# Kernel tuning notes

Hardware: AMD Instinct MI355X
Metric: run time of the kernel (lower is better)

Reference implementation:

```python
import jax, jax.numpy as jnp
import numpy as np

N_EMBD = 1024
N_HEAD = 16
HEAD_DIM = N_EMBD // N_HEAD


def setup_inputs() -> dict:
    key = jax.random.key(0)
    ks = jax.random.split(key, 5)
    B, T, C = 2, 2048, N_EMBD
    scale = 0.02
    return {
        "x": jax.random.normal(ks[0], (B, T, C), dtype=jnp.float32),
        "w_attn": jax.random.normal(ks[1], (C, 3 * C), dtype=jnp.float32) * scale,
        "b_attn": jax.random.normal(ks[2], (3 * C,), dtype=jnp.float32) * scale,
        "w_proj": jax.random.normal(ks[3], (C, C), dtype=jnp.float32) * scale,
        "b_proj": jax.random.normal(ks[4], (C,), dtype=jnp.float32) * scale,
    }


def reference(x, w_attn, b_attn, w_proj, b_proj):
    B, T, C = x.shape
    H, D = N_HEAD, HEAD_DIM
    qkv = x @ w_attn + b_attn  # [B,T,3C]
    q, k, v = jnp.split(qkv, 3, axis=-1)
    # [B,T,C] -> [B,H,T,D]
    q = q.reshape(B, T, H, D).transpose(0, 2, 1, 3)
    k = k.reshape(B, T, H, D).transpose(0, 2, 1, 3)
    v = v.reshape(B, T, H, D).transpose(0, 2, 1, 3)
    scores = jnp.einsum("bhqd,bhkd->bhqk", q, k) / jnp.sqrt(jnp.float32(D))
    causal = jnp.tril(jnp.ones((T, T), dtype=bool))
    scores = jnp.where(causal, scores, jnp.finfo(scores.dtype).min)
    attn = jax.nn.softmax(scores, axis=-1)
    y = jnp.einsum("bhqk,bhkd->bhqd", attn, v)  # [B,H,T,D]
    y = y.transpose(0, 2, 1, 3).reshape(B, T, C)
    return y @ w_proj + b_proj
```

## Files before the change

### kernel.cpp

```cpp
#include <hip/hip_runtime.h>

typedef unsigned short u16;
typedef u16 u16x4 __attribute__((ext_vector_type(4)));
typedef u16 u16x8 __attribute__((ext_vector_type(8)));
typedef __bf16 bf16x8 __attribute__((ext_vector_type(8)));
typedef float floatx4 __attribute__((ext_vector_type(4)));

#define N_EMBD 1024
#define N_HEAD 16
#define HEAD_DIM 64
#define SEQ 2048
#define BATCH 2
#define M_ROWS (BATCH * SEQ)

typedef __attribute__((address_space(1))) const unsigned char ga_t;
typedef __attribute__((address_space(3))) unsigned char la_t;

#if __has_builtin(__builtin_amdgcn_exp2f)
#define EXP2(x) __builtin_amdgcn_exp2f(x)
#else
#define EXP2(x) exp2f(x)
#endif

__device__ __forceinline__ u16 cvt_bf16(float f) {
  return __builtin_bit_cast(u16, (__bf16)f);
}

__global__ __launch_bounds__(256) void prep(const float* __restrict__ x,
                                            u16* __restrict__ xb,
                                            const float* __restrict__ wa,
                                            const float* __restrict__ wp,
                                            u16* __restrict__ outa,
                                            u16* __restrict__ outp) {
  const int bid = blockIdx.x;
  if (bid < 2048) {
    const long i = ((long)bid * 256 + threadIdx.x) * 8;
    const float4 f0 = *(const float4*)&x[i];
    const float4 f1 = *(const float4*)&x[i + 4];
    u16x8 p;
    p[0] = cvt_bf16(f0.x); p[1] = cvt_bf16(f0.y);
    p[2] = cvt_bf16(f0.z); p[3] = cvt_bf16(f0.w);
    p[4] = cvt_bf16(f1.x); p[5] = cvt_bf16(f1.y);
    p[6] = cvt_bf16(f1.z); p[7] = cvt_bf16(f1.w);
    *(u16x8*)&xb[i] = p;
    return;
  }
  __shared__ u16 tile[32][33];
  const int t = bid - 2048;
  const int gx = t & 127;
  const int gy = t >> 7;
  const int R = N_EMBD;
  const float* in;
  u16* out;
  int C, bx;
  if (gx < 96) {
    in = wa; out = outa; C = 3 * N_EMBD; bx = gx * 32;
  } else {
    in = wp; out = outp; C = N_EMBD; bx = (gx - 96) * 32;
  }
  const int by = gy * 32;
  const int tx = threadIdx.x & 31;
  const int ty = threadIdx.x >> 5;
#pragma unroll
  for (int j = 0; j < 32; j += 8)
    tile[ty + j][tx] = cvt_bf16(in[(long)(by + ty + j) * C + bx + tx]);
  __syncthreads();
#pragma unroll
  for (int j = 0; j < 32; j += 8)
    out[(long)(bx + ty + j) * R + by + tx] = tile[tx][ty + j];
}

#define BK 32

template <int MODE>
__device__ __forceinline__ void stage128(const u16* __restrict__ A,
                                         const u16* __restrict__ Bt, int bm,
                                         int bn, int kt, int K, int tid,
                                         u16* as, u16* bs) {
  const int w = tid >> 6;
  const int l = tid & 63;
  const int lrow = l >> 2;
#pragma unroll
  for (int p = 0; p < 2; ++p) {
    const int arow = p * 64 + w * 16;
    const int row = arow + lrow;
    const int sl = (l & 3) ^ ((row >> 1) & 3);
    long gA;
    if (MODE == 0) {
      gA = (long)(bm + row) * K + kt + sl * 8;
    } else {
      const int m = bm + row;
      const int b = m >> 11, t = m & 2047;
      const int k0 = kt + sl * 8;
      const int head = k0 >> 6, dd = k0 & 63;
      gA = (((long)(b * N_HEAD + head)) * SEQ + t) * HEAD_DIM + dd;
    }
    __builtin_amdgcn_global_load_lds((ga_t*)(A + gA), (la_t*)&as[arow * BK],
                                     16, 0, 0);
    const long gB = (long)(bn + row) * K + kt + sl * 8;
    __builtin_amdgcn_global_load_lds((ga_t*)(Bt + gB), (la_t*)&bs[arow * BK],
                                     16, 0, 0);
  }
}

template <int MODE>
__global__ __launch_bounds__(256) void gemm128(
    const u16* __restrict__ A, const u16* __restrict__ Bt,
    const float* __restrict__ bias, float* __restrict__ out,
    u16* __restrict__ qo, u16* __restrict__ ko, u16* __restrict__ vo, int N,
    int K) {
  __shared__ u16 As[2][128 * BK];
  __shared__ u16 Bs[2][128 * BK];
  const int tid = threadIdx.x;

  const int nx = gridDim.x;
  const int nwg = nx * gridDim.y;
  int lin = blockIdx.y * nx + blockIdx.x;
  lin = (lin & 7) * (nwg >> 3) + (lin >> 3);
  const int bm = (lin / nx) * 128;
  const int bn = (lin % nx) * 128;

  const int w = tid >> 6;
  const int l = tid & 63;
  const int wm = (w >> 1) * 64;
  const int wn = (w & 1) * 64;
  const int m16 = l & 15;
  const int quad = l >> 4;
  const int ksw = (quad ^ ((m16 >> 1) & 3)) * 8;

  floatx4 acc[4][4];
#pragma unroll
  for (int i = 0; i < 4; ++i)
#pragma unroll
    for (int j = 0; j < 4; ++j) acc[i][j] = (floatx4){0.f, 0.f, 0.f, 0.f};

  const int nk = K / BK;
  stage128<MODE>(A, Bt, bm, bn, 0, K, tid, As[0], Bs[0]);
  __syncthreads();

  int cur = 0;
  for (int t = 0; t < nk; ++t) {
    if (t + 1 < nk)
      stage128<MODE>(A, Bt, bm, bn, (t + 1) * BK, K, tid, As[cur ^ 1],
                     Bs[cur ^ 1]);

    bf16x8 af[4], bfr[4];
#pragma unroll
    for (int i = 0; i < 4; ++i)
      af[i] = __builtin_bit_cast(
          bf16x8, *(const u16x8*)&As[cur][(wm + i * 16 + m16) * BK + ksw]);
#pragma unroll
    for (int j = 0; j < 4; ++j)
      bfr[j] = __builtin_bit_cast(
          bf16x8, *(const u16x8*)&Bs[cur][(wn + j * 16 + m16) * BK + ksw]);
#pragma unroll
    for (int i = 0; i < 4; ++i)
#pragma unroll
      for (int j = 0; j < 4; ++j)
        acc[i][j] = __builtin_amdgcn_mfma_f32_16x16x32_bf16(af[i], bfr[j],
                                                            acc[i][j], 0, 0, 0);
    __syncthreads();
    cur ^= 1;
  }

#pragma unroll
  for (int i = 0; i < 4; ++i) {
#pragma unroll
    for (int j = 0; j < 4; ++j) {
      const int col = bn + wn + j * 16 + m16;
      const float bv = bias[col];
      if (MODE == 1) {
#pragma unroll
        for (int r = 0; r < 4; ++r) {
          const int row = bm + wm + i * 16 + quad * 4 + r;
          out[(long)row * N_EMBD + col] = acc[i][j][r] + bv;
        }
      } else {
        const int which = col >> 10;
        const int cc = col & 1023;
        const int h = cc >> 6;
        const int dd = cc & 63;
        const int row0 = bm + wm + i * 16 + quad * 4;
        const int b = row0 >> 11;
        const int t0 = row0 & 2047;
        if (which == 2) {
          u16x4 pk;
#pragma unroll
          for (int r = 0; r < 4; ++r) pk[r] = cvt_bf16(acc[i][j][r] + bv);
          *(u16x4*)&vo[(((long)(b * N_HEAD + h)) * HEAD_DIM + dd) * SEQ + t0] =
              pk;
        } else {
          u16* dst = (which == 0) ? qo : ko;
#pragma unroll
          for (int r = 0; r < 4; ++r)
            dst[(((long)(b * N_HEAD + h)) * SEQ + t0 + r) * HEAD_DIM + dd] =
                cvt_bf16(acc[i][j][r] + bv);
        }
      }
    }
  }
}

#define BQ 64
#define BKV 64
#define LOG2E 1.44269504f
#define NQT (SEQ / BQ)

__device__ __forceinline__ void stage_kv(const u16* __restrict__ K,
                                         const u16* __restrict__ Vt, long bh,
                                         int kt, int tid, u16* kl, u16* vl) {
#pragma unroll
  for (int i = 0; i < 2; ++i) {
    const int p = tid + 256 * i;
    const int row = p >> 3;
    const int slot = (p & 7) ^ (row & 7);
    const int wb = (i * 256 + (tid & 192)) * 8;
    __builtin_amdgcn_global_load_lds(
        (ga_t*)&K[(bh * SEQ + kt + row) * HEAD_DIM + slot * 8], (la_t*)&kl[wb],
        16, 0, 0);
    __builtin_amdgcn_global_load_lds(
        (ga_t*)&Vt[(bh * HEAD_DIM + row) * SEQ + kt + slot * 8], (la_t*)&vl[wb],
        16, 0, 0);
  }
}

__global__ __launch_bounds__(256, 4) void flash_attn(
    u16* __restrict__ Qy, const u16* __restrict__ K,
    const u16* __restrict__ Vt) {
  const int id = blockIdx.x;
  const int iq = (NQT - 1) - (id >> 5);
  const int bh_ = ((id >> 3) & 3) * 8 + (id & 7);
  const long bh = bh_;
  const int tid = threadIdx.x;
  const int w = tid >> 6;
  const int l = tid & 63;
  const int m16 = l & 15;
  const int quad = l >> 4;

  __shared__ u16 Kl[2][BKV * 64];
  __shared__ u16 Vl[2][64 * BKV];
  __shared__ u16 Pl[4][16 * 64];

  const float SC = 0.125f * LOG2E;
  const int qb = iq * BQ;
  const int ntiles = iq + 1;
  const int qglob = qb + w * 16 + m16;
  const int sw = (m16 & 7) << 3;

  bf16x8 qf[2];
  {
    const u16* qrow = Qy + (bh * SEQ + qglob) * HEAD_DIM;
    qf[0] = __builtin_bit_cast(bf16x8, *(const u16x8*)&qrow[quad * 8]);
    qf[1] = __builtin_bit_cast(bf16x8, *(const u16x8*)&qrow[32 + quad * 8]);
  }

  floatx4 Oacc[4];
#pragma unroll
  for (int t = 0; t < 4; ++t) Oacc[t] = (floatx4){0.f, 0.f, 0.f, 0.f};
  float mrow = -1e30f, lrow = 0.f;

  stage_kv(K, Vt, bh, 0, tid, Kl[0], Vl[0]);
  __syncthreads();

  for (int it = 0; it < ntiles; ++it) {
    const int buf = it & 1;
    const int kt = it * BKV;
    if (it + 1 < ntiles)
      stage_kv(K, Vt, bh, kt + BKV, tid, Kl[buf ^ 1], Vl[buf ^ 1]);

    floatx4 s[4];
#pragma unroll
    for (int j = 0; j < 4; ++j) s[j] = (floatx4){0.f, 0.f, 0.f, 0.f};
#pragma unroll
    for (int j = 0; j < 4; ++j)
#pragma unroll
      for (int kk = 0; kk < 2; ++kk) {
        const bf16x8 kf = __builtin_bit_cast(
            bf16x8, *(const u16x8*)&Kl[buf][(j * 16 + m16) * 64 +
                                            ((kk * 32 + quad * 8) ^ sw)]);
        s[j] = __builtin_amdgcn_mfma_f32_16x16x32_bf16(kf, qf[kk], s[j], 0, 0,
                                                       0);
      }
    if (it == ntiles - 1) {
#pragma unroll
      for (int j = 0; j < 4; ++j) {
        const int key0 = kt + j * 16 + quad * 4;
#pragma unroll
        for (int r = 0; r < 4; ++r)
          if (key0 + r > qglob) s[j][r] = -1e30f;
      }
    }

    float t0 = fmaxf(fmaxf(s[0][0], s[0][1]), fmaxf(s[0][2], s[0][3]));
    float t1 = fmaxf(fmaxf(s[1][0], s[1][1]), fmaxf(s[1][2], s[1][3]));
    float t2 = fmaxf(fmaxf(s[2][0], s[2][1]), fmaxf(s[2][2], s[2][3]));
    float t3 = fmaxf(fmaxf(s[3][0], s[3][1]), fmaxf(s[3][2], s[3][3]));
    float tm = fmaxf(fmaxf(t0, t1), fmaxf(t2, t3));
    tm = fmaxf(tm, __shfl_xor(tm, 16, 64));
    tm = fmaxf(tm, __shfl_xor(tm, 32, 64));
    const float pm = tm * SC;
    if (!__all(pm <= mrow + 4.f)) {
      const float mn = fmaxf(mrow, pm);
      const float al = EXP2(mrow - mn);
      mrow = mn;
      lrow *= al;
#pragma unroll
      for (int t = 0; t < 4; ++t)
#pragma unroll
        for (int r = 0; r < 4; ++r) Oacc[t][r] *= al;
    }

    float ls = 0.f;
#pragma unroll
    for (int j = 0; j < 4; ++j) {
      u16x4 pk;
#pragma unroll
      for (int r = 0; r < 4; ++r) {
        const float p = EXP2(__builtin_fmaf(s[j][r], SC, -mrow));
        ls += p;
        pk[r] = cvt_bf16(p);
      }
      *(u16x4*)&Pl[w][m16 * 64 + ((j * 16 + quad * 4) ^ sw)] = pk;
    }
    ls += __shfl_xor(ls, 16, 64);
    ls += __shfl_xor(ls, 32, 64);
    lrow += ls;

    bf16x8 pf[2];
    pf[0] = __builtin_bit_cast(
        bf16x8, *(const u16x8*)&Pl[w][m16 * 64 + ((quad * 8) ^ sw)]);
    pf[1] = __builtin_bit_cast(
        bf16x8, *(const u16x8*)&Pl[w][m16 * 64 + ((32 + quad * 8) ^ sw)]);
#pragma unroll
    for (int t = 0; t < 4; ++t)
#pragma unroll
      for (int kk = 0; kk < 2; ++kk) {
        const bf16x8 vf = __builtin_bit_cast(
            bf16x8, *(const u16x8*)&Vl[buf][(t * 16 + m16) * 64 +
                                            ((kk * 32 + quad * 8) ^ sw)]);
        Oacc[t] = __builtin_amdgcn_mfma_f32_16x16x32_bf16(vf, pf[kk], Oacc[t],
                                                          0, 0, 0);
      }
    __syncthreads();
  }

  const float invl = 1.f / lrow;
#pragma unroll
  for (int t = 0; t < 4; ++t) {
    u16x4 pk;
#pragma unroll
    for (int r = 0; r < 4; ++r) pk[r] = cvt_bf16(Oacc[t][r] * invl);
    *(u16x4*)&Qy[(bh * SEQ + qglob) * HEAD_DIM + t * 16 + quad * 4] = pk;
  }
}

extern "C" void kernel_launch(void* const* d_in, const int* in_sizes, int n_in,
                              void* d_out, int out_size, void* d_ws,
                              size_t ws_size, hipStream_t stream) {
  const float* x = (const float*)d_in[0];
  const float* w_attn = (const float*)d_in[1];
  const float* b_attn = (const float*)d_in[2];
  const float* w_proj = (const float*)d_in[3];
  const float* b_proj = (const float*)d_in[4];
  float* out = (float*)d_out;

  char* ws = (char*)d_ws;
  const size_t SZ = (size_t)BATCH * N_HEAD * SEQ * HEAD_DIM * sizeof(u16);
  u16* q = (u16*)(ws);
  u16* k = (u16*)(ws + SZ);
  u16* vT = (u16*)(ws + 2 * SZ);
  u16* wT_a = (u16*)(ws + 3 * SZ);
  u16* wT_p = (u16*)(ws + 3 * SZ + (size_t)3 * N_EMBD * N_EMBD * sizeof(u16));
  u16* xb = (u16*)(ws + 3 * SZ + (size_t)4 * N_EMBD * N_EMBD * sizeof(u16));

  prep<<<2048 + 4096, 256, 0, stream>>>(x, xb, w_attn, w_proj, wT_a, wT_p);

  gemm128<0><<<dim3(3 * N_EMBD / 128, M_ROWS / 128), 256, 0, stream>>>(
      xb, wT_a, b_attn, nullptr, q, k, vT, 3 * N_EMBD, N_EMBD);

  flash_attn<<<NQT * 32, 256, 0, stream>>>(q, k, vT);

  gemm128<1><<<dim3(N_EMBD / 128, M_ROWS / 128), 256, 0, stream>>>(
      q, wT_p, b_proj, out, nullptr, nullptr, nullptr, N_EMBD, N_EMBD);
}
```

Measured before the change: 182.1 us.

## Double flash-attention query tile to 128 with 8 waves sharing K/V tiles

Raises the attention query block from 64 to 128 rows, runs 8 waves per 512-thread block, and has each thread stage one 16-byte chunk of K and V, so each K/V tile loaded into LDS is reused by twice as many query rows. Block scheduling changes from strictly longest-first to an order that interleaves long and short causal tiles. Masking now starts at a per-wave tile index. The cost is fewer, larger blocks with more LDS and registers per block, plus some wasted work on the diagonal tiles for waves whose rows fall in the lower half.

```diff
diff --git a/kernel.cpp b/kernel.cpp
--- a/kernel.cpp
+++ b/kernel.cpp
@@ -201,7 +201,7 @@
   }
 }
 
-#define BQ 64
+#define BQ 128
 #define BKV 64
 #define LOG2E 1.44269504f
 #define NQT (SEQ / BQ)
@@ -209,28 +209,24 @@
 __device__ __forceinline__ void stage_kv(const u16* __restrict__ K,
                                          const u16* __restrict__ Vt, long bh,
                                          int kt, int tid, u16* kl, u16* vl) {
-#pragma unroll
-  for (int i = 0; i < 2; ++i) {
-    const int p = tid + 256 * i;
-    const int row = p >> 3;
-    const int slot = (p & 7) ^ (row & 7);
-    const int wb = (i * 256 + (tid & 192)) * 8;
-    __builtin_amdgcn_global_load_lds(
-        (ga_t*)&K[(bh * SEQ + kt + row) * HEAD_DIM + slot * 8], (la_t*)&kl[wb],
-        16, 0, 0);
-    __builtin_amdgcn_global_load_lds(
-        (ga_t*)&Vt[(bh * HEAD_DIM + row) * SEQ + kt + slot * 8], (la_t*)&vl[wb],
-        16, 0, 0);
-  }
-}
-
-__global__ __launch_bounds__(256, 4) void flash_attn(
+  const int row = tid >> 3;
+  const int slot = (tid & 7) ^ (row & 7);
+  const int wb = (tid & 448) * 8;
+  __builtin_amdgcn_global_load_lds(
+      (ga_t*)&K[(bh * SEQ + kt + row) * HEAD_DIM + slot * 8], (la_t*)&kl[wb],
+      16, 0, 0);
+  __builtin_amdgcn_global_load_lds(
+      (ga_t*)&Vt[(bh * HEAD_DIM + row) * SEQ + kt + slot * 8], (la_t*)&vl[wb],
+      16, 0, 0);
+}
+
+__global__ __launch_bounds__(512, 6) void flash_attn(
     u16* __restrict__ Qy, const u16* __restrict__ K,
     const u16* __restrict__ Vt) {
   const int id = blockIdx.x;
-  const int iq = (NQT - 1) - (id >> 5);
-  const int bh_ = ((id >> 3) & 3) * 8 + (id & 7);
-  const long bh = bh_;
+  const int o = id >> 5;
+  const int j = (o < 8) ? (15 - o) : (o - 8);
+  const long bh = id & 31;
   const int tid = threadIdx.x;
   const int w = tid >> 6;
   const int l = tid & 63;
@@ -239,12 +235,13 @@
 
   __shared__ u16 Kl[2][BKV * 64];
   __shared__ u16 Vl[2][64 * BKV];
-  __shared__ u16 Pl[4][16 * 64];
+  __shared__ u16 Pl[8][16 * 64];
 
   const float SC = 0.125f * LOG2E;
-  const int qb = iq * BQ;
-  const int ntiles = iq + 1;
+  const int qb = j * BQ;
+  const int ntiles = 2 * j + 2;
   const int qglob = qb + w * 16 + m16;
+  const int maskstart = (qb + w * 16) >> 6;
   const int sw = (m16 & 7) << 3;
 
   bf16x8 qf[2];
@@ -270,24 +267,24 @@
 
     floatx4 s[4];
 #pragma unroll
-    for (int j = 0; j < 4; ++j) s[j] = (floatx4){0.f, 0.f, 0.f, 0.f};
-#pragma unroll
-    for (int j = 0; j < 4; ++j)
+    for (int jj = 0; jj < 4; ++jj) s[jj] = (floatx4){0.f, 0.f, 0.f, 0.f};
+#pragma unroll
+    for (int jj = 0; jj < 4; ++jj)
 #pragma unroll
       for (int kk = 0; kk < 2; ++kk) {
         const bf16x8 kf = __builtin_bit_cast(
-            bf16x8, *(const u16x8*)&Kl[buf][(j * 16 + m16) * 64 +
+            bf16x8, *(const u16x8*)&Kl[buf][(jj * 16 + m16) * 64 +
                                             ((kk * 32 + quad * 8) ^ sw)]);
-        s[j] = __builtin_amdgcn_mfma_f32_16x16x32_bf16(kf, qf[kk], s[j], 0, 0,
-                                                       0);
-      }
-    if (it == ntiles - 1) {
-#pragma unroll
-      for (int j = 0; j < 4; ++j) {
-        const int key0 = kt + j * 16 + quad * 4;
+        s[jj] = __builtin_amdgcn_mfma_f32_16x16x32_bf16(kf, qf[kk], s[jj], 0,
+                                                        0, 0);
+      }
+    if (it >= maskstart) {
+#pragma unroll
+      for (int jj = 0; jj < 4; ++jj) {
+        const int key0 = kt + jj * 16 + quad * 4;
 #pragma unroll
         for (int r = 0; r < 4; ++r)
-          if (key0 + r > qglob) s[j][r] = -1e30f;
+          if (key0 + r > qglob) s[jj][r] = -1e30f;
       }
     }
 
@@ -312,15 +309,15 @@
 
     float ls = 0.f;
 #pragma unroll
-    for (int j = 0; j < 4; ++j) {
+    for (int jj = 0; jj < 4; ++jj) {
       u16x4 pk;
 #pragma unroll
       for (int r = 0; r < 4; ++r) {
-        const float p = EXP2(__builtin_fmaf(s[j][r], SC, -mrow));
+        const float p = EXP2(__builtin_fmaf(s[jj][r], SC, -mrow));
         ls += p;
         pk[r] = cvt_bf16(p);
       }
-      *(u16x4*)&Pl[w][m16 * 64 + ((j * 16 + quad * 4) ^ sw)] = pk;
+      *(u16x4*)&Pl[w][m16 * 64 + ((jj * 16 + quad * 4) ^ sw)] = pk;
     }
     ls += __shfl_xor(ls, 16, 64);
     ls += __shfl_xor(ls, 32, 64);
@@ -378,7 +375,7 @@
   gemm128<0><<<dim3(3 * N_EMBD / 128, M_ROWS / 128), 256, 0, stream>>>(
       xb, wT_a, b_attn, nullptr, q, k, vT, 3 * N_EMBD, N_EMBD);
 
-  flash_attn<<<NQT * 32, 256, 0, stream>>>(q, k, vT);
+  flash_attn<<<NQT * 32, 512, 0, stream>>>(q, k, vT);
 
   gemm128<1><<<dim3(N_EMBD / 128, M_ROWS / 128), 256, 0, stream>>>(
       q, wT_p, b_proj, out, nullptr, nullptr, nullptr, N_EMBD, N_EMBD);
```

New measurement: 190.5 us. +4.6%, slower.
